# Kernel optimization log

Measured on AMD Instinct MI355X. Metric: run time of the kernel, lower is better.

## Reference

```python
import jax, jax.numpy as jnp
import numpy as np
from jax import lax

B, CIN, COUT, H, W, K = 256, 512, 256, 8, 8, 8192


def setup_inputs() -> dict:
    key = jax.random.key(0)
    ks = jax.random.split(key, 6)
    scale = 0.05
    return {
        "latent": jax.random.normal(ks[0], (B, CIN, H, W), dtype=jnp.float32),
        "conv_w": jax.random.normal(ks[1], (COUT, CIN, 3, 3), dtype=jnp.float32) * scale,
        "conv_b": jax.random.normal(ks[2], (COUT,), dtype=jnp.float32) * scale,
        "lin_w": jax.random.normal(ks[3], (COUT, COUT), dtype=jnp.float32) * scale,
        "lin_b": jax.random.normal(ks[4], (COUT,), dtype=jnp.float32) * scale,
        "emb": jax.random.normal(ks[5], (K, COUT), dtype=jnp.float32),
    }


def reference(latent, conv_w, conv_b, lin_w, lin_b, emb):
    # pre-quantization conv: 3x3, stride 1, padding 1 (SAME), NCHW / OIHW
    x = lax.conv_general_dilated(
        latent, conv_w, window_strides=(1, 1), padding="SAME",
        dimension_numbers=("NCHW", "OIHW", "NCHW"),
    ) + conv_b[None, :, None, None]
    # permute(0,2,3,1) then linear on last dim
    x = jnp.transpose(x, (0, 2, 3, 1))              # [B,H,W,C]
    x = jnp.einsum("bhwc,dc->bhwd", x, lin_w) + lin_b
    flat = x.reshape(-1, x.shape[-1])               # [B*H*W, C]
    distances = (
        jnp.sum(flat ** 2, axis=1, keepdims=True)
        + jnp.sum(emb ** 2, axis=1)
        - 2.0 * flat @ emb.T
    )                                               # [B*H*W, K]
    encoding_indices = jnp.argmin(distances, axis=1)
    return encoding_indices.reshape(-1, 64)
```

## Files before the change

kernel.cpp:

```cpp
#include <hip/hip_runtime.h>
#include <cstdint>
#include <cstddef>


#define CIN_  512
#define E_    4608
#define M_    16384

typedef _Float16 half4_t __attribute__((ext_vector_type(4)));
typedef _Float16 half8_t __attribute__((ext_vector_type(8)));
typedef float f32x4 __attribute__((ext_vector_type(4)));

#define GLOAD_LDS16(gptr, lptr)                                         \
    __builtin_amdgcn_global_load_lds(                                   \
        (const __attribute__((address_space(1))) unsigned int*)(gptr),  \
        (__attribute__((address_space(3))) unsigned int*)(lptr), 16, 0, 0)

__global__ void tkern(const float* __restrict__ src, float* __restrict__ dst,
                      int R, int C) {
    __shared__ float t[32][33];
    int c = blockIdx.x * 32 + threadIdx.x;
    int r = blockIdx.y * 32 + threadIdx.y;
    if (r < R && c < C) t[threadIdx.y][threadIdx.x] = src[(size_t)r * C + c];
    __syncthreads();
    int rr = blockIdx.x * 32 + threadIdx.y;
    int cc = blockIdx.y * 32 + threadIdx.x;
    if (rr < C && cc < R) dst[(size_t)rr * R + cc] = t[threadIdx.x][threadIdx.y];
}

__global__ __launch_bounds__(256) void fold5_k(const float* __restrict__ conv_w,
                                               const float* __restrict__ lwT,
                                               _Float16* __restrict__ W2x) {
    int e0 = blockIdx.x * 8;
    int d = threadIdx.x;
    float acc[8];
    #pragma unroll
    for (int j = 0; j < 8; ++j) acc[j] = 0.f;
    for (int co = 0; co < 256; ++co) {
        float lw = lwT[co * 256 + d];
        const float* cwr = conv_w + (size_t)co * E_ + e0;
        #pragma unroll
        for (int j = 0; j < 8; ++j) acc[j] += cwr[j] * lw;
    }
    #pragma unroll
    for (int j = 0; j < 8; ++j) {
        int e = e0 + j;
        int c = e / 9, t9 = e - c * 9;
        _Float16 h = (_Float16)acc[j];
        _Float16 l = (_Float16)(acc[j] - (float)h);
        W2x[((size_t)(t9 * 256 + d)) * 512 + c] = h;
        W2x[((size_t)((9 + t9) * 256 + d)) * 512 + c] = l;
    }
}

__global__ void bias_k(const float* __restrict__ lwT, const float* __restrict__ conv_b,
                       const float* __restrict__ lin_b, float* __restrict__ b2) {
    int d = threadIdx.x;
    float acc = lin_b[d];
    for (int co = 0; co < 256; ++co) acc += lwT[co * 256 + d] * conv_b[co];
    b2[d] = acc;
}

__global__ void embsq_k(const float* __restrict__ emb, float* __restrict__ esq) {
    int w = threadIdx.x >> 6, lane = threadIdx.x & 63;
    int k = blockIdx.x * 4 + w;
    const float* row = emb + (size_t)k * 256;
    float s = 0.f;
    #pragma unroll
    for (int i = 0; i < 4; ++i) { float v = row[lane + 64 * i]; s += v * v; }
    #pragma unroll
    for (int m = 32; m >= 1; m >>= 1) s += __shfl_xor(s, m, 64);
    if (lane == 0) esq[k] = s;
}

__global__ __launch_bounds__(256) void packlat_k(const float* __restrict__ lat,
                                                 _Float16* __restrict__ Xnp) {
    int b = blockIdx.x, t = threadIdx.x;
    __shared__ float lt[128][65];
    const float* src = lat + (size_t)b * 512 * 64;
    _Float16* dst = Xnp + (size_t)b * 64 * 1024;
    for (int c0 = 0; c0 < 512; c0 += 128) {
        __syncthreads();
        #pragma unroll
        for (int j = 0; j < 8; ++j) {
            int f4 = t + j * 256;
            int cc = f4 >> 4, p4 = (f4 & 15) * 4;
            float4 v = *(const float4*)(src + (size_t)(c0 + cc) * 64 + p4);
            lt[cc][p4] = v.x; lt[cc][p4 + 1] = v.y;
            lt[cc][p4 + 2] = v.z; lt[cc][p4 + 3] = v.w;
        }
        __syncthreads();
        int pix = t >> 2, cr = (t & 3) * 32;
        #pragma unroll
        for (int q = 0; q < 4; ++q) {
            half8_t hh, ll;
            #pragma unroll
            for (int j = 0; j < 8; ++j) {
                float v = lt[cr + q * 8 + j][pix];
                _Float16 h = (_Float16)v;
                hh[j] = h; ll[j] = (_Float16)(v - (float)h);
            }
            *(half8_t*)(dst + (size_t)pix * 1024 + c0 + cr + q * 8) = hh;
            *(half8_t*)(dst + (size_t)pix * 1024 + 512 + c0 + cr + q * 8) = ll;
        }
    }
}

__global__ __launch_bounds__(256) void convm4_k(
    const _Float16* __restrict__ Xnp, const _Float16* __restrict__ W2x,
    const float* __restrict__ b2, const _Float16* __restrict__ zp,
    float* __restrict__ yb) {
    __shared__ char sm[65536];
    int m0 = blockIdx.x * 128, n0 = blockIdx.y * 128;
    int tid = threadIdx.x, w = tid >> 6, lane = tid & 63;
    int wm = w & 1, wn = w >> 1;
    int fr = lane & 15, fq = lane >> 4;

    int xq = (fq ^ ((fr >> 1) & 3)) << 4;
    int aoff[4], boff[4];
    #pragma unroll
    for (int i = 0; i < 4; ++i) {
        aoff[i] = (wm * 64 + i * 16 + fr) * 64 + xq;
        boff[i] = (wn * 64 + i * 16 + fr) * 64 + xq;
    }
    int slt[2], sr[2], sq[2];
    #pragma unroll
    for (int i = 0; i < 2; ++i) {
        int s = w * 128 + i * 64 + lane;
        slt[i] = s;
        sr[i] = s >> 2;
        sq[i] = ((s & 3) ^ ((s >> 3) & 3)) * 8;
    }

    f32x4 acc[4][4];
    #pragma unroll
    for (int s = 0; s < 4; ++s)
        #pragma unroll
        for (int t = 0; t < 4; ++t)
            #pragma unroll
            for (int r = 0; r < 4; ++r) acc[s][t][r] = 0.f;

    auto stage = [&](int it, int buf) {
        int tap = it >> 4, cc = it & 15;
        int dy = tap / 3 - 1, dx = tap - (tap / 3) * 3 - 1;
        char* L = sm + buf * 32768;
        #pragma unroll
        for (int i = 0; i < 2; ++i) {
            int choff = cc * 32 + sq[i];
            int gm = m0 + sr[i];
            int img = gm >> 6, pix = gm & 63;
            int ih = (pix >> 3) + dy, iw = (pix & 7) + dx;
            bool v = ((unsigned)ih < 8u) && ((unsigned)iw < 8u);
            const _Float16* a0 = v
                ? Xnp + ((size_t)(img * 64 + ih * 8 + iw)) * 1024 : zp;
            const _Float16* a1 = v ? a0 + 512 : zp;
            GLOAD_LDS16(a0 + choff, L + slt[i] * 16);
            GLOAD_LDS16(a1 + choff, L + 8192 + slt[i] * 16);
            const _Float16* bb =
                W2x + ((size_t)(tap * 256 + n0 + sr[i])) * 512 + choff;
            GLOAD_LDS16(bb, L + 16384 + slt[i] * 16);
            GLOAD_LDS16(bb + (size_t)9 * 256 * 512, L + 24576 + slt[i] * 16);
        }
    };

    stage(0, 0);
    for (int it = 0; it < 144; ++it) {
        __syncthreads();
        if (it + 1 < 144) stage(it + 1, (it + 1) & 1);
        const char* L = sm + (it & 1) * 32768;
        half8_t ah[4], al[4], bh[4], bl[4];
        #pragma unroll
        for (int s = 0; s < 4; ++s) ah[s] = *(const half8_t*)(L + aoff[s]);
        #pragma unroll
        for (int t = 0; t < 4; ++t) bh[t] = *(const half8_t*)(L + 16384 + boff[t]);
        #pragma unroll
        for (int s = 0; s < 4; ++s)
            #pragma unroll
            for (int t = 0; t < 4; ++t)
                acc[s][t] = __builtin_amdgcn_mfma_f32_16x16x32_f16(
                    ah[s], bh[t], acc[s][t], 0, 0, 0);
        #pragma unroll
        for (int t = 0; t < 4; ++t) bl[t] = *(const half8_t*)(L + 24576 + boff[t]);
        #pragma unroll
        for (int s = 0; s < 4; ++s)
            #pragma unroll
            for (int t = 0; t < 4; ++t)
                acc[s][t] = __builtin_amdgcn_mfma_f32_16x16x32_f16(
                    ah[s], bl[t], acc[s][t], 0, 0, 0);
        #pragma unroll
        for (int s = 0; s < 4; ++s) al[s] = *(const half8_t*)(L + 8192 + aoff[s]);
        #pragma unroll
        for (int s = 0; s < 4; ++s)
            #pragma unroll
            for (int t = 0; t < 4; ++t)
                acc[s][t] = __builtin_amdgcn_mfma_f32_16x16x32_f16(
                    al[s], bh[t], acc[s][t], 0, 0, 0);
    }

    float bv[4];
    #pragma unroll
    for (int t = 0; t < 4; ++t) bv[t] = b2[n0 + wn * 64 + t * 16 + fr];
    #pragma unroll
    for (int s = 0; s < 4; ++s)
        #pragma unroll
        for (int r = 0; r < 4; ++r) {
            int m = m0 + wm * 64 + s * 16 + fq * 4 + r;
            #pragma unroll
            for (int t = 0; t < 4; ++t) {
                int d = n0 + wn * 64 + t * 16 + fr;
                yb[(size_t)m * 256 + d] = acc[s][t][r] + bv[t];
            }
        }
}

__global__ void packhi_k(const float* __restrict__ x, _Float16* __restrict__ o) {
    int i = blockIdx.x * 256 + threadIdx.x;
    float4 v = *(const float4*)(x + (size_t)i * 4);
    half4_t h = {(_Float16)v.x, (_Float16)v.y, (_Float16)v.z, (_Float16)v.w};
    *(half4_t*)(o + (size_t)i * 4) = h;
}

__global__ __launch_bounds__(256) void screen4_k(
    const _Float16* __restrict__ A2, const _Float16* __restrict__ B2,
    const float* __restrict__ esq, float* __restrict__ ps2, int* __restrict__ pi2) {
    __shared__ char sm[65536];
    int m0 = blockIdx.x * 128, n0 = blockIdx.y * 128;
    int tid = threadIdx.x, w = tid >> 6, lane = tid & 63;
    int wm = w & 1, wn = w >> 1;
    int fr = lane & 15, fq = lane >> 4;

    int xq8[2];
    #pragma unroll
    for (int kk = 0; kk < 2; ++kk) xq8[kk] = ((kk * 4 + fq) ^ (fr & 7)) << 4;
    int arow[4], brow[4];
    #pragma unroll
    for (int i = 0; i < 4; ++i) {
        arow[i] = (wm * 64 + i * 16 + fr) * 128;
        brow[i] = (wn * 64 + i * 16 + fr) * 128;
    }
    int slt[4], sr[4], sq[4];
    #pragma unroll
    for (int i = 0; i < 4; ++i) {
        int s = w * 256 + i * 64 + lane;
        slt[i] = s;
        sr[i] = s >> 3;
        sq[i] = ((s & 7) ^ ((s >> 3) & 7)) * 8;
    }

    auto stage = [&](int kt, int buf) {
        char* L = sm + buf * 32768;
        int ko = kt * 64;
        #pragma unroll
        for (int i = 0; i < 4; ++i) {
            GLOAD_LDS16(A2 + (size_t)(m0 + sr[i]) * 256 + ko + sq[i],
                        L + slt[i] * 16);
            GLOAD_LDS16(B2 + (size_t)(n0 + sr[i]) * 256 + ko + sq[i],
                        L + 16384 + slt[i] * 16);
        }
    };

    f32x4 acc[4][4];
    #pragma unroll
    for (int s = 0; s < 4; ++s)
        #pragma unroll
        for (int t = 0; t < 4; ++t)
            #pragma unroll
            for (int r = 0; r < 4; ++r) acc[s][t][r] = 0.f;

    stage(0, 0);
    for (int kt = 0; kt < 4; ++kt) {
        __syncthreads();
        if (kt + 1 < 4) stage(kt + 1, (kt + 1) & 1);
        const char* L = sm + (kt & 1) * 32768;
        #pragma unroll
        for (int kk = 0; kk < 2; ++kk) {
            half8_t af[4], bf[4];
            #pragma unroll
            for (int s = 0; s < 4; ++s)
                af[s] = *(const half8_t*)(L + arow[s] + xq8[kk]);
            #pragma unroll
            for (int t = 0; t < 4; ++t)
                bf[t] = *(const half8_t*)(L + 16384 + brow[t] + xq8[kk]);
            #pragma unroll
            for (int s = 0; s < 4; ++s)
                #pragma unroll
                for (int t = 0; t < 4; ++t)
                    acc[s][t] = __builtin_amdgcn_mfma_f32_16x16x32_f16(
                        af[s], bf[t], acc[s][t], 0, 0, 0);
        }
    }

    float esv[4];
    #pragma unroll
    for (int t = 0; t < 4; ++t) esv[t] = esq[n0 + wn * 64 + t * 16 + fr];
    int colIdx = blockIdx.y * 2 + wn;
    #pragma unroll
    for (int s = 0; s < 4; ++s) {
        #pragma unroll
        for (int r = 0; r < 4; ++r) {
            float best = 3.4e38f; int bidx = 0x7fffffff;
            #pragma unroll
            for (int t = 0; t < 4; ++t) {
                float sc = esv[t] - 2.f * acc[s][t][r];
                int k = n0 + wn * 64 + t * 16 + fr;
                if (sc < best || (sc == best && k < bidx)) { best = sc; bidx = k; }
            }
            #pragma unroll
            for (int msk = 1; msk <= 8; msk <<= 1) {
                float so = __shfl_xor(best, msk, 64);
                int ko2 = __shfl_xor(bidx, msk, 64);
                if (so < best || (so == best && ko2 < bidx)) { best = so; bidx = ko2; }
            }
            if (fr == 0) {
                int m = m0 + wm * 64 + s * 16 + fq * 4 + r;
                ps2[(size_t)m * 128 + colIdx] = best;
                pi2[(size_t)m * 128 + colIdx] = bidx;
            }
        }
    }
}

__global__ __launch_bounds__(256) void refine2_k(
    const float* __restrict__ y, const float* __restrict__ emb,
    const float* __restrict__ esq, const float* __restrict__ ps2,
    const int* __restrict__ pi2, int* __restrict__ out) {
    int lane = threadIdx.x & 63;
    int m = blockIdx.x * 4 + (threadIdx.x >> 6);
    float4 yv = *(const float4*)(y + (size_t)m * 256 + lane * 4);
    float sc_[2]; int kc_[2];
    #pragma unroll
    for (int i = 0; i < 2; ++i) {
        sc_[i] = ps2[(size_t)m * 128 + lane * 2 + i];
        kc_[i] = pi2[(size_t)m * 128 + lane * 2 + i];
    }
    float s0 = fminf(sc_[0], sc_[1]);
    #pragma unroll
    for (int msk = 1; msk <= 32; msk <<= 1) s0 = fminf(s0, __shfl_xor(s0, msk, 64));
    float thr = s0 + 0.25f;
    float best = 3.4e38f; int bk = 0x7fffffff;
    for (int c = 0; c < 128; ++c) {
        float scc = __shfl(sc_[c & 1], c >> 1, 64);
        if (scc <= thr) {
            int k = __shfl(kc_[c & 1], c >> 1, 64);
            float4 ev = *(const float4*)(emb + (size_t)k * 256 + lane * 4);
            float d = yv.x * ev.x + yv.y * ev.y + yv.z * ev.z + yv.w * ev.w;
            #pragma unroll
            for (int msk = 1; msk <= 32; msk <<= 1) d += __shfl_xor(d, msk, 64);
            float sx = esq[k] - 2.f * d;
            if (sx < best || (sx == best && k < bk)) { best = sx; bk = k; }
        }
    }
    if (lane == 0) out[m] = bk;
}

extern "C" void kernel_launch(void* const* d_in, const int* in_sizes, int n_in,
                              void* d_out, int out_size, void* d_ws, size_t ws_size,
                              hipStream_t stream) {
    const float* latent = (const float*)d_in[0];
    const float* conv_w = (const float*)d_in[1];
    const float* conv_b = (const float*)d_in[2];
    const float* lin_w  = (const float*)d_in[3];
    const float* lin_b  = (const float*)d_in[4];
    const float* emb    = (const float*)d_in[5];
    int* out = (int*)d_out;

    char* W = (char*)d_ws;
    float*    lwT = (float*)(W + 0);
    float*    b2  = (float*)(W + 262144);
    float*    esq = (float*)(W + 263168);
    float*    yb  = (float*)(W + 295936);
    _Float16* W2x = (_Float16*)(W + 17073152);
    _Float16* zp  = (_Float16*)(W + 21791744);
    _Float16* Xnp = (_Float16*)(W + 21792768);
    _Float16* A2  = (_Float16*)(W + 21792768);
    _Float16* B2  = (_Float16*)(W + 30181376);
    float*    ps2 = (float*)(W + 34375680);
    int*      pi2 = (int*)(W + 42764288);

    dim3 t32(32, 32);
    tkern<<<dim3(8, 8), t32, 0, stream>>>(lin_w, lwT, 256, 256);
    bias_k<<<1, 256, 0, stream>>>(lwT, conv_b, lin_b, b2);
    embsq_k<<<2048, 256, 0, stream>>>(emb, esq);
    fold5_k<<<576, 256, 0, stream>>>(conv_w, lwT, W2x);
    hipMemsetAsync(zp, 0, 1024, stream);
    packlat_k<<<256, 256, 0, stream>>>(latent, Xnp);

    convm4_k<<<dim3(128, 2), 256, 0, stream>>>(Xnp, W2x, b2, zp, yb);

    packhi_k<<<4096, 256, 0, stream>>>(yb, A2);
    packhi_k<<<2048, 256, 0, stream>>>(emb, B2);
    screen4_k<<<dim3(128, 64), 256, 0, stream>>>(A2, B2, esq, ps2, pi2);
    refine2_k<<<4096, 256, 0, stream>>>(yb, emb, esq, ps2, pi2, out);
}
```

Before: 520.7 us.

## Make screen kernel persistent with A tile held in registers across codebook tiles

The screening GEMM now runs as 512 persistent blocks. Each block loads its 128-row A tile once into LDS and registers, then streams 16 codebook tiles of B through a double buffer. Per-tile argmin reduction is done inline, which removes the redundant A reloads and launch overhead of the 8192-block grid. The helper kernels (embsq, packhi, refine) are also changed to grid-stride style with 512 blocks. In exchange, occupancy drops to one block per CU with 96KB of dynamic LDS, and register pressure rises from holding 32 A fragments.

Result: slower. 652.0 us (+25.2%).

```diff
diff --git a/kernel.cpp b/kernel.cpp
--- a/kernel.cpp
+++ b/kernel.cpp
@@ -61,16 +61,19 @@
     b2[d] = acc;
 }
 
-__global__ void embsq_k(const float* __restrict__ emb, float* __restrict__ esq) {
+__global__ void embsq2_k(const float* __restrict__ emb, float* __restrict__ esq) {
     int w = threadIdx.x >> 6, lane = threadIdx.x & 63;
-    int k = blockIdx.x * 4 + w;
-    const float* row = emb + (size_t)k * 256;
-    float s = 0.f;
-    #pragma unroll
-    for (int i = 0; i < 4; ++i) { float v = row[lane + 64 * i]; s += v * v; }
-    #pragma unroll
-    for (int m = 32; m >= 1; m >>= 1) s += __shfl_xor(s, m, 64);
-    if (lane == 0) esq[k] = s;
+    #pragma unroll
+    for (int it = 0; it < 4; ++it) {
+        int k = (blockIdx.x + it * 512) * 4 + w;
+        const float* row = emb + (size_t)k * 256;
+        float s = 0.f;
+        #pragma unroll
+        for (int i = 0; i < 4; ++i) { float v = row[lane + 64 * i]; s += v * v; }
+        #pragma unroll
+        for (int m = 32; m >= 1; m >>= 1) s += __shfl_xor(s, m, 64);
+        if (lane == 0) esq[k] = s;
+    }
 }
 
 __global__ __launch_bounds__(256) void packlat_k(const float* __restrict__ lat,
@@ -213,31 +216,27 @@
         }
 }
 
-__global__ void packhi_k(const float* __restrict__ x, _Float16* __restrict__ o) {
-    int i = blockIdx.x * 256 + threadIdx.x;
-    float4 v = *(const float4*)(x + (size_t)i * 4);
-    half4_t h = {(_Float16)v.x, (_Float16)v.y, (_Float16)v.z, (_Float16)v.w};
-    *(half4_t*)(o + (size_t)i * 4) = h;
-}
-
-__global__ __launch_bounds__(256) void screen4_k(
+__global__ void packhi_s(const float* __restrict__ x, _Float16* __restrict__ o,
+                         int iters) {
+    for (int it = 0; it < iters; ++it) {
+        int i = (blockIdx.x + it * 512) * 256 + threadIdx.x;
+        float4 v = *(const float4*)(x + (size_t)i * 4);
+        half4_t h = {(_Float16)v.x, (_Float16)v.y, (_Float16)v.z, (_Float16)v.w};
+        *(half4_t*)(o + (size_t)i * 4) = h;
+    }
+}
+
+#define SCR_LDS 98304
+__global__ __launch_bounds__(256, 1) void screen5_k(
     const _Float16* __restrict__ A2, const _Float16* __restrict__ B2,
     const float* __restrict__ esq, float* __restrict__ ps2, int* __restrict__ pi2) {
-    __shared__ char sm[65536];
-    int m0 = blockIdx.x * 128, n0 = blockIdx.y * 128;
+    extern __shared__ char sm[];
+    int mt = blockIdx.x >> 2, ng = blockIdx.x & 3;
+    int m0 = mt * 128;
     int tid = threadIdx.x, w = tid >> 6, lane = tid & 63;
     int wm = w & 1, wn = w >> 1;
     int fr = lane & 15, fq = lane >> 4;
 
-    int xq8[2];
-    #pragma unroll
-    for (int kk = 0; kk < 2; ++kk) xq8[kk] = ((kk * 4 + fq) ^ (fr & 7)) << 4;
-    int arow[4], brow[4];
-    #pragma unroll
-    for (int i = 0; i < 4; ++i) {
-        arow[i] = (wm * 64 + i * 16 + fr) * 128;
-        brow[i] = (wn * 64 + i * 16 + fr) * 128;
-    }
     int slt[4], sr[4], sq[4];
     #pragma unroll
     for (int i = 0; i < 4; ++i) {
@@ -246,18 +245,44 @@
         sr[i] = s >> 3;
         sq[i] = ((s & 7) ^ ((s >> 3) & 7)) * 8;
     }
-
-    auto stage = [&](int kt, int buf) {
-        char* L = sm + buf * 32768;
-        int ko = kt * 64;
-        #pragma unroll
-        for (int i = 0; i < 4; ++i) {
-            GLOAD_LDS16(A2 + (size_t)(m0 + sr[i]) * 256 + ko + sq[i],
-                        L + slt[i] * 16);
-            GLOAD_LDS16(B2 + (size_t)(n0 + sr[i]) * 256 + ko + sq[i],
-                        L + 16384 + slt[i] * 16);
-        }
+    int xq8[2];
+    #pragma unroll
+    for (int kk = 0; kk < 2; ++kk) xq8[kk] = ((kk * 4 + fq) ^ (fr & 7)) << 4;
+    int arow[4], brow[4];
+    #pragma unroll
+    for (int i = 0; i < 4; ++i) {
+        arow[i] = (wm * 64 + i * 16 + fr) * 128;
+        brow[i] = (wn * 64 + i * 16 + fr) * 128;
+    }
+
+    #pragma unroll
+    for (int kt = 0; kt < 4; ++kt)
+        #pragma unroll
+        for (int i = 0; i < 4; ++i)
+            GLOAD_LDS16(A2 + (size_t)(m0 + sr[i]) * 256 + kt * 64 + sq[i],
+                        sm + kt * 16384 + slt[i] * 16);
+
+    char* Bb = sm + 65536;
+    auto stageB = [&](int q) {
+        int j = q >> 2, kt = q & 3, buf = q & 1;
+        int n0 = (ng * 16 + j) * 128;
+        #pragma unroll
+        for (int i = 0; i < 4; ++i)
+            GLOAD_LDS16(B2 + (size_t)(n0 + sr[i]) * 256 + kt * 64 + sq[i],
+                        Bb + buf * 16384 + slt[i] * 16);
     };
+    stageB(0);
+    __syncthreads();
+
+    half8_t af[4][8];
+    #pragma unroll
+    for (int kt = 0; kt < 4; ++kt)
+        #pragma unroll
+        for (int kk = 0; kk < 2; ++kk)
+            #pragma unroll
+            for (int s = 0; s < 4; ++s)
+                af[s][kt * 2 + kk] =
+                    *(const half8_t*)(sm + kt * 16384 + arow[s] + xq8[kk]);
 
     f32x4 acc[4][4];
     #pragma unroll
@@ -267,90 +292,101 @@
             #pragma unroll
             for (int r = 0; r < 4; ++r) acc[s][t][r] = 0.f;
 
-    stage(0, 0);
-    for (int kt = 0; kt < 4; ++kt) {
-        __syncthreads();
-        if (kt + 1 < 4) stage(kt + 1, (kt + 1) & 1);
-        const char* L = sm + (kt & 1) * 32768;
-        #pragma unroll
-        for (int kk = 0; kk < 2; ++kk) {
-            half8_t af[4], bf[4];
-            #pragma unroll
-            for (int s = 0; s < 4; ++s)
-                af[s] = *(const half8_t*)(L + arow[s] + xq8[kk]);
+    float esv[4];
+    for (int j = 0; j < 16; ++j) {
+        int n0 = (ng * 16 + j) * 128;
+        #pragma unroll
+        for (int kt = 0; kt < 4; ++kt) {
+            int q = j * 4 + kt;
+            __syncthreads();
+            if (q + 1 < 64) stageB(q + 1);
+            if (kt == 0) {
+                #pragma unroll
+                for (int t = 0; t < 4; ++t)
+                    esv[t] = esq[n0 + wn * 64 + t * 16 + fr];
+            }
+            const char* L = Bb + (q & 1) * 16384;
+            #pragma unroll
+            for (int kk = 0; kk < 2; ++kk) {
+                half8_t bf[4];
+                #pragma unroll
+                for (int t = 0; t < 4; ++t)
+                    bf[t] = *(const half8_t*)(L + brow[t] + xq8[kk]);
+                #pragma unroll
+                for (int s = 0; s < 4; ++s)
+                    #pragma unroll
+                    for (int t = 0; t < 4; ++t)
+                        acc[s][t] = __builtin_amdgcn_mfma_f32_16x16x32_f16(
+                            af[s][kt * 2 + kk], bf[t], acc[s][t], 0, 0, 0);
+            }
+        }
+        int colIdx = (ng * 16 + j) * 2 + wn;
+        #pragma unroll
+        for (int s = 0; s < 4; ++s) {
+            #pragma unroll
+            for (int r = 0; r < 4; ++r) {
+                float best = 3.4e38f; int bidx = 0x7fffffff;
+                #pragma unroll
+                for (int t = 0; t < 4; ++t) {
+                    float sc = esv[t] - 2.f * acc[s][t][r];
+                    int k = n0 + wn * 64 + t * 16 + fr;
+                    if (sc < best || (sc == best && k < bidx)) { best = sc; bidx = k; }
+                }
+                #pragma unroll
+                for (int msk = 1; msk <= 8; msk <<= 1) {
+                    float so = __shfl_xor(best, msk, 64);
+                    int ko2 = __shfl_xor(bidx, msk, 64);
+                    if (so < best || (so == best && ko2 < bidx)) { best = so; bidx = ko2; }
+                }
+                if (fr == 0) {
+                    int m = m0 + wm * 64 + s * 16 + fq * 4 + r;
+                    ps2[(size_t)m * 128 + colIdx] = best;
+                    pi2[(size_t)m * 128 + colIdx] = bidx;
+                }
+            }
+        }
+        #pragma unroll
+        for (int s = 0; s < 4; ++s)
             #pragma unroll
             for (int t = 0; t < 4; ++t)
-                bf[t] = *(const half8_t*)(L + 16384 + brow[t] + xq8[kk]);
-            #pragma unroll
-            for (int s = 0; s < 4; ++s)
-                #pragma unroll
-                for (int t = 0; t < 4; ++t)
-                    acc[s][t] = __builtin_amdgcn_mfma_f32_16x16x32_f16(
-                        af[s], bf[t], acc[s][t], 0, 0, 0);
-        }
-    }
-
-    float esv[4];
-    #pragma unroll
-    for (int t = 0; t < 4; ++t) esv[t] = esq[n0 + wn * 64 + t * 16 + fr];
-    int colIdx = blockIdx.y * 2 + wn;
-    #pragma unroll
-    for (int s = 0; s < 4; ++s) {
-        #pragma unroll
-        for (int r = 0; r < 4; ++r) {
-            float best = 3.4e38f; int bidx = 0x7fffffff;
-            #pragma unroll
-            for (int t = 0; t < 4; ++t) {
-                float sc = esv[t] - 2.f * acc[s][t][r];
-                int k = n0 + wn * 64 + t * 16 + fr;
-                if (sc < best || (sc == best && k < bidx)) { best = sc; bidx = k; }
-            }
-            #pragma unroll
-            for (int msk = 1; msk <= 8; msk <<= 1) {
-                float so = __shfl_xor(best, msk, 64);
-                int ko2 = __shfl_xor(bidx, msk, 64);
-                if (so < best || (so == best && ko2 < bidx)) { best = so; bidx = ko2; }
-            }
-            if (fr == 0) {
-                int m = m0 + wm * 64 + s * 16 + fq * 4 + r;
-                ps2[(size_t)m * 128 + colIdx] = best;
-                pi2[(size_t)m * 128 + colIdx] = bidx;
-            }
-        }
-    }
-}
-
-__global__ __launch_bounds__(256) void refine2_k(
+                #pragma unroll
+                for (int r = 0; r < 4; ++r) acc[s][t][r] = 0.f;
+    }
+}
+
+__global__ __launch_bounds__(256) void refine3_k(
     const float* __restrict__ y, const float* __restrict__ emb,
     const float* __restrict__ esq, const float* __restrict__ ps2,
     const int* __restrict__ pi2, int* __restrict__ out) {
     int lane = threadIdx.x & 63;
-    int m = blockIdx.x * 4 + (threadIdx.x >> 6);
-    float4 yv = *(const float4*)(y + (size_t)m * 256 + lane * 4);
-    float sc_[2]; int kc_[2];
-    #pragma unroll
-    for (int i = 0; i < 2; ++i) {
-        sc_[i] = ps2[(size_t)m * 128 + lane * 2 + i];
-        kc_[i] = pi2[(size_t)m * 128 + lane * 2 + i];
-    }
-    float s0 = fminf(sc_[0], sc_[1]);
-    #pragma unroll
-    for (int msk = 1; msk <= 32; msk <<= 1) s0 = fminf(s0, __shfl_xor(s0, msk, 64));
-    float thr = s0 + 0.25f;
-    float best = 3.4e38f; int bk = 0x7fffffff;
-    for (int c = 0; c < 128; ++c) {
-        float scc = __shfl(sc_[c & 1], c >> 1, 64);
-        if (scc <= thr) {
-            int k = __shfl(kc_[c & 1], c >> 1, 64);
-            float4 ev = *(const float4*)(emb + (size_t)k * 256 + lane * 4);
-            float d = yv.x * ev.x + yv.y * ev.y + yv.z * ev.z + yv.w * ev.w;
-            #pragma unroll
-            for (int msk = 1; msk <= 32; msk <<= 1) d += __shfl_xor(d, msk, 64);
-            float sx = esq[k] - 2.f * d;
-            if (sx < best || (sx == best && k < bk)) { best = sx; bk = k; }
-        }
-    }
-    if (lane == 0) out[m] = bk;
+    for (int j = 0; j < 8; ++j) {
+        int m = blockIdx.x * 32 + j * 4 + (threadIdx.x >> 6);
+        float4 yv = *(const float4*)(y + (size_t)m * 256 + lane * 4);
+        float sc_[2]; int kc_[2];
+        #pragma unroll
+        for (int i = 0; i < 2; ++i) {
+            sc_[i] = ps2[(size_t)m * 128 + lane * 2 + i];
+            kc_[i] = pi2[(size_t)m * 128 + lane * 2 + i];
+        }
+        float s0 = fminf(sc_[0], sc_[1]);
+        #pragma unroll
+        for (int msk = 1; msk <= 32; msk <<= 1) s0 = fminf(s0, __shfl_xor(s0, msk, 64));
+        float thr = s0 + 0.25f;
+        float best = 3.4e38f; int bk = 0x7fffffff;
+        for (int c = 0; c < 128; ++c) {
+            float scc = __shfl(sc_[c & 1], c >> 1, 64);
+            if (scc <= thr) {
+                int k = __shfl(kc_[c & 1], c >> 1, 64);
+                float4 ev = *(const float4*)(emb + (size_t)k * 256 + lane * 4);
+                float d = yv.x * ev.x + yv.y * ev.y + yv.z * ev.z + yv.w * ev.w;
+                #pragma unroll
+                for (int msk = 1; msk <= 32; msk <<= 1) d += __shfl_xor(d, msk, 64);
+                float sx = esq[k] - 2.f * d;
+                if (sx < best || (sx == best && k < bk)) { best = sx; bk = k; }
+            }
+        }
+        if (lane == 0) out[m] = bk;
+    }
 }
 
 extern "C" void kernel_launch(void* const* d_in, const int* in_sizes, int n_in,
@@ -380,15 +416,15 @@
     dim3 t32(32, 32);
     tkern<<<dim3(8, 8), t32, 0, stream>>>(lin_w, lwT, 256, 256);
     bias_k<<<1, 256, 0, stream>>>(lwT, conv_b, lin_b, b2);
-    embsq_k<<<2048, 256, 0, stream>>>(emb, esq);
+    embsq2_k<<<512, 256, 0, stream>>>(emb, esq);
     fold5_k<<<576, 256, 0, stream>>>(conv_w, lwT, W2x);
     hipMemsetAsync(zp, 0, 1024, stream);
     packlat_k<<<256, 256, 0, stream>>>(latent, Xnp);
 
     convm4_k<<<dim3(128, 2), 256, 0, stream>>>(Xnp, W2x, b2, zp, yb);
 
-    packhi_k<<<4096, 256, 0, stream>>>(yb, A2);
-    packhi_k<<<2048, 256, 0, stream>>>(emb, B2);
-    screen4_k<<<dim3(128, 64), 256, 0, stream>>>(A2, B2, esq, ps2, pi2);
-    refine2_k<<<4096, 256, 0, stream>>>(yb, emb, esq, ps2, pi2, out);
-}
+    packhi_s<<<512, 256, 0, stream>>>(yb, A2, 8);
+    packhi_s<<<512, 256, 0, stream>>>(emb, B2, 4);
+    screen5_k<<<512, 256, SCR_LDS, stream>>>(A2, B2, esq, ps2, pi2);
+    refine3_k<<<512, 256, 0, stream>>>(yb, emb, esq, ps2, pi2, out);
+}
```
